# Kernel tuning notes

Hardware: AMD Instinct MI355X
Metric: run time of the kernel (lower is better)

Reference implementation:

```python
import jax, jax.numpy as jnp
import numpy as np

N_NODES = 50000
N_EDGES = 1600000
D_FEAT = 128
ORDER = 2


def setup_inputs() -> dict:
    key = jax.random.key(0)
    k1, k2, k3, k4 = jax.random.split(key, 4)
    x = jax.random.normal(k1, (N_NODES, D_FEAT), dtype=jnp.float32)
    adj_row = jax.random.randint(k2, (N_EDGES,), 0, N_NODES, dtype=jnp.int32)
    adj_col = jax.random.randint(k3, (N_EDGES,), 0, N_NODES, dtype=jnp.int32)
    adj_vals = jax.random.uniform(k4, (N_EDGES,), dtype=jnp.float32)
    return {"x": x, "adj_row": adj_row, "adj_col": adj_col, "adj_vals": adj_vals}


def reference(x, adj_row, adj_col, adj_vals):
    # SGC propagation: x <- A @ x, repeated `order` times.
    # A is sparse COO: A[row, col] = vals; spmm(A, x)[i] = sum_e vals[e]*x[col[e]] into row[e].
    for _ in range(ORDER):
        msgs = adj_vals[:, None] * x[adj_col]          # [E, F] gathered messages
        x = jax.ops.segment_sum(msgs, adj_row, num_segments=N_NODES)  # [N, F]
    return x
```

## Files before the change

### kernel.cpp

```cpp
#include <hip/hip_runtime.h>
#include <hip/hip_fp16.h>

#define N_NODES 50000
#define N_EDGES 1600000
#define D_FEAT  128
#define NB      ((N_NODES + 255) >> 8)

#define P1_WGS   400
#define P1_ROUND 4096
#define P1_CAP   38
#define P2_CAP   14336

__device__ __forceinline__ unsigned short f2bf(float f) {
    union { float f; unsigned u; } v; v.f = f;
    unsigned r = v.u + 0x7fff + ((v.u >> 16) & 1);
    return (unsigned short)(r >> 16);
}
__device__ __forceinline__ float bf_lo(unsigned w) {
    union { unsigned u; float f; } v; v.u = w << 16; return v.f;
}
__device__ __forceinline__ float bf_hi(unsigned w) {
    union { unsigned u; float f; } v; v.u = w & 0xffff0000u; return v.f;
}

__global__ __launch_bounds__(256) void coarse_hist_kernel(
    const int* __restrict__ row, int* __restrict__ gcnt)
{
    __shared__ int s_cnt[NB];
    for (int i = threadIdx.x; i < NB; i += 256) s_cnt[i] = 0;
    __syncthreads();
    int stride = gridDim.x * blockDim.x;
    for (int e = blockIdx.x * blockDim.x + threadIdx.x; e < N_EDGES; e += stride)
        atomicAdd(&s_cnt[row[e] >> 8], 1);
    __syncthreads();
    for (int i = threadIdx.x; i < NB; i += 256)
        if (s_cnt[i]) atomicAdd(&gcnt[i], s_cnt[i]);
}

__global__ __launch_bounds__(256) void bucket_scan_kernel(
    const int* __restrict__ gcnt, int* __restrict__ gbase,
    int* __restrict__ gcur, int* __restrict__ row_ptr)
{
    __shared__ int lds[256];
    int t = threadIdx.x;
    int orig = (t < NB) ? gcnt[t] : 0;
    lds[t] = orig;
    __syncthreads();
    for (int off = 1; off < 256; off <<= 1) {
        int u = (t >= off) ? lds[t - off] : 0;
        __syncthreads();
        lds[t] += u;
        __syncthreads();
    }
    int excl = lds[t] - orig;
    if (t < NB) { gbase[t] = excl; gcur[t] = excl; }
    if (t == 0) row_ptr[N_NODES] = N_EDGES;
}

__global__ __launch_bounds__(256) void p1_bin_kernel(
    const int* __restrict__ row, const int* __restrict__ col,
    const float* __restrict__ val,
    int* __restrict__ gcur, uint2* __restrict__ sedge)
{
    __shared__ uint2    s_buf[NB * P1_CAP];
    __shared__ unsigned s_cnt[NB];
    __shared__ int      s_base[NB];

    int wg = blockIdx.x, t = threadIdx.x;
    int e0 = (int)((long)wg * N_EDGES / P1_WGS);
    int e1 = (int)((long)(wg + 1) * N_EDGES / P1_WGS);

    for (int rbase = e0; rbase < e1; rbase += P1_ROUND) {
        int rend = rbase + P1_ROUND; if (rend > e1) rend = e1;
        for (int i = t; i < NB; i += 256) s_cnt[i] = 0;
        __syncthreads();
        for (int e = rbase + t; e < rend; e += 256) {
            int r = row[e];
            int b = r >> 8;
            uint2 rec;
            rec.x = ((unsigned)r << 16) | (unsigned)col[e];
            rec.y = __float_as_uint(val[e]);
            unsigned pos = atomicAdd(&s_cnt[b], 1u);
            if (pos < P1_CAP) {
                s_buf[b * P1_CAP + pos] = rec;
            } else {
                int gp = atomicAdd(&gcur[b], 1);
                sedge[gp] = rec;
            }
        }
        __syncthreads();
        if (t < NB) {
            int c = (int)s_cnt[t]; if (c > P1_CAP) c = P1_CAP;
            s_base[t] = (c > 0) ? atomicAdd(&gcur[t], c) : 0;
        }
        __syncthreads();
        if (t < NB) {
            int c = (int)s_cnt[t]; if (c > P1_CAP) c = P1_CAP;
            int gb = s_base[t];
            for (int i = 0; i < c; ++i)
                sedge[gb + i] = s_buf[t * P1_CAP + i];
        }
        __syncthreads();
    }
}

__global__ __launch_bounds__(256) void p2_sort_kernel(
    const int* __restrict__ gbase, const int* __restrict__ gcur,
    const uint2* __restrict__ sedge,
    unsigned* __restrict__ spair, int* __restrict__ row_ptr)
{
    __shared__ unsigned s_out[P2_CAP];
    __shared__ int s_cnt[256];
    __shared__ int s_cur[256];

    int b = blockIdx.x, t = threadIdx.x;
    int beg = gbase[b];
    int end = gcur[b];
    int cnt = end - beg;
    int row0 = b << 8;

    s_cnt[t] = 0;
    __syncthreads();
    for (int i = beg + t; i < end; i += 256) {
        int fr = (int)(sedge[i].x >> 16) - row0;
        atomicAdd(&s_cnt[fr], 1);
    }
    __syncthreads();
    int orig = s_cnt[t];
    __syncthreads();
    for (int off = 1; off < 256; off <<= 1) {
        int u = (t >= off) ? s_cnt[t - off] : 0;
        __syncthreads();
        s_cnt[t] += u;
        __syncthreads();
    }
    int excl = s_cnt[t] - orig;
    int r = row0 + t;
    if (r < N_NODES) row_ptr[r] = beg + excl;
    s_cur[t] = excl;
    __syncthreads();

    if (cnt <= P2_CAP) {
        for (int i = beg + t; i < end; i += 256) {
            uint2 rec = sedge[i];
            int fr = (int)(rec.x >> 16) - row0;
            int p = atomicAdd(&s_cur[fr], 1);
            unsigned cv = rec.x & 0xffffu;
            unsigned short hv = __half_as_ushort(__float2half(__uint_as_float(rec.y)));
            s_out[p] = (cv << 16) | (unsigned)hv;
        }
        __syncthreads();
        for (int i = t; i < cnt; i += 256)
            spair[beg + i] = s_out[i];
    } else {
        for (int i = beg + t; i < end; i += 256) {
            uint2 rec = sedge[i];
            int fr = (int)(rec.x >> 16) - row0;
            int p = atomicAdd(&s_cur[fr], 1);
            unsigned cv = rec.x & 0xffffu;
            unsigned short hv = __half_as_ushort(__float2half(__uint_as_float(rec.y)));
            spair[beg + p] = (cv << 16) | (unsigned)hv;
        }
    }
}

__global__ __launch_bounds__(256) void conv_kernel(
    const float2* __restrict__ xin, unsigned* __restrict__ xb)
{
    int t = blockIdx.x * blockDim.x + threadIdx.x;
    if (t < N_NODES * (D_FEAT / 2)) {
        float2 f = xin[t];
        xb[t] = ((unsigned)f2bf(f.y) << 16) | (unsigned)f2bf(f.x);
    }
}

template <bool WRITE_BF16>
__global__ __launch_bounds__(256) void spmm_csr_bf_kernel(
    const int*      __restrict__ row_ptr,
    const unsigned* __restrict__ spair,
    const unsigned* __restrict__ xb,
    unsigned* __restrict__ outb,
    float*    __restrict__ outf)
{
    int group = (blockIdx.x * blockDim.x + threadIdx.x) >> 4;
    int lane  = threadIdx.x & 15;
    if (group >= N_NODES) return;

    int start = row_ptr[group];
    int end   = row_ptr[group + 1];

    float acc[8];
    #pragma unroll
    for (int i = 0; i < 8; ++i) acc[i] = 0.f;

    for (int base = start; base < end; base += 16) {
        int n = end - base; if (n > 16) n = 16;
        int   c = 0;
        float v = 0.f;
        if (lane < n) {
            unsigned rec = spair[base + lane];
            c = (int)(rec >> 16);
            v = __half2float(__ushort_as_half((unsigned short)(rec & 0xffffu)));
        }
        for (int j = 0; j < n; ++j) {
            int   cj = __shfl(c, j, 16);
            float vj = __shfl(v, j, 16);
            uint4 w = *(const uint4*)(xb + (long)cj * (D_FEAT / 2) + lane * 4);
            acc[0] += vj * bf_lo(w.x);
            acc[1] += vj * bf_hi(w.x);
            acc[2] += vj * bf_lo(w.y);
            acc[3] += vj * bf_hi(w.y);
            acc[4] += vj * bf_lo(w.z);
            acc[5] += vj * bf_hi(w.z);
            acc[6] += vj * bf_lo(w.w);
            acc[7] += vj * bf_hi(w.w);
        }
    }

    if (WRITE_BF16) {
        uint4 w;
        w.x = ((unsigned)f2bf(acc[1]) << 16) | (unsigned)f2bf(acc[0]);
        w.y = ((unsigned)f2bf(acc[3]) << 16) | (unsigned)f2bf(acc[2]);
        w.z = ((unsigned)f2bf(acc[5]) << 16) | (unsigned)f2bf(acc[4]);
        w.w = ((unsigned)f2bf(acc[7]) << 16) | (unsigned)f2bf(acc[6]);
        *(uint4*)(outb + (long)group * (D_FEAT / 2) + lane * 4) = w;
    } else {
        float4 a = make_float4(acc[0], acc[1], acc[2], acc[3]);
        float4 b = make_float4(acc[4], acc[5], acc[6], acc[7]);
        float* dst = outf + (long)group * D_FEAT + lane * 8;
        *(float4*)(dst + 0) = a;
        *(float4*)(dst + 4) = b;
    }
}

__global__ __launch_bounds__(256) void spmm_atomic_kernel(
    const int* __restrict__ row, const int* __restrict__ col,
    const float* __restrict__ vals, const float* __restrict__ xin,
    float* __restrict__ xout)
{
    long tid   = (long)blockIdx.x * blockDim.x + threadIdx.x;
    int  edge  = (int)(tid >> 5);
    int  chunk = (int)(tid & 31);
    if (edge >= N_EDGES) return;
    int   r = row[edge];
    int   c = col[edge];
    float v = vals[edge];
    const float4 xv = ((const float4*)(xin + (long)c * D_FEAT))[chunk];
    float* dst = xout + (long)r * D_FEAT + chunk * 4;
    unsafeAtomicAdd(dst + 0, v * xv.x);
    unsafeAtomicAdd(dst + 1, v * xv.y);
    unsafeAtomicAdd(dst + 2, v * xv.z);
    unsafeAtomicAdd(dst + 3, v * xv.w);
}

static inline size_t align_up(size_t x, size_t a) { return (x + a - 1) & ~(a - 1); }

extern "C" void kernel_launch(void* const* d_in, const int* in_sizes, int n_in,
                              void* d_out, int out_size, void* d_ws, size_t ws_size,
                              hipStream_t stream) {
    const float* x        = (const float*)d_in[0];
    const int*   adj_row  = (const int*)d_in[1];
    const int*   adj_col  = (const int*)d_in[2];
    const float* adj_vals = (const float*)d_in[3];
    float*       out      = (float*)d_out;

    const size_t bf_bytes = (size_t)N_NODES * (D_FEAT / 2) * sizeof(unsigned);

    char*     ws      = (char*)d_ws;
    size_t    off     = 0;
    unsigned* xb      = (unsigned*)(ws + off); off = align_up(off + bf_bytes, 512);
    unsigned* tmpb    = (unsigned*)(ws + off); off = align_up(off + bf_bytes, 512);
    uint2*    sedge   = (uint2*)   (ws + off); off = align_up(off + (size_t)N_EDGES * 8, 512);
    unsigned* spair   = (unsigned*)(ws + off); off = align_up(off + (size_t)N_EDGES * 4, 512);
    int*      row_ptr = (int*)     (ws + off); off = align_up(off + (N_NODES + 4) * sizeof(int), 512);
    int*      gcnt    = (int*)     (ws + off); off = align_up(off + NB * sizeof(int), 512);
    int*      gbase   = (int*)     (ws + off); off = align_up(off + NB * sizeof(int), 512);
    int*      gcur    = (int*)     (ws + off); off = align_up(off + NB * sizeof(int), 512);
    const size_t needed = off;

    const int block = 256;

    if (ws_size >= needed) {
        hipMemsetAsync(gcnt, 0, NB * sizeof(int), stream);
        coarse_hist_kernel<<<256, block, 0, stream>>>(adj_row, gcnt);
        bucket_scan_kernel<<<1, block, 0, stream>>>(gcnt, gbase, gcur, row_ptr);
        p1_bin_kernel<<<P1_WGS, block, 0, stream>>>(adj_row, adj_col, adj_vals,
                                                    gcur, sedge);
        p2_sort_kernel<<<NB, block, 0, stream>>>(gbase, gcur, sedge, spair, row_ptr);

        int cgrid = (N_NODES * (D_FEAT / 2) + block - 1) / block;
        conv_kernel<<<cgrid, block, 0, stream>>>((const float2*)x, xb);

        int ngrid = (N_NODES * 16 + block - 1) / block;
        spmm_csr_bf_kernel<true><<<ngrid, block, 0, stream>>>(
            row_ptr, spair, xb, tmpb, (float*)nullptr);
        spmm_csr_bf_kernel<false><<<ngrid, block, 0, stream>>>(
            row_ptr, spair, tmpb, (unsigned*)nullptr, out);
    } else {
        float* tmp = (float*)ws;
        const size_t feat_bytes = (size_t)N_NODES * D_FEAT * sizeof(float);
        hipMemsetAsync(tmp, 0, feat_bytes, stream);
        hipMemsetAsync(out, 0, feat_bytes, stream);
        long total_threads = (long)N_EDGES * 32;
        long grid = (total_threads + block - 1) / block;
        spmm_atomic_kernel<<<dim3((unsigned)grid), dim3(block), 0, stream>>>(
            adj_row, adj_col, adj_vals, x, tmp);
        spmm_atomic_kernel<<<dim3((unsigned)grid), dim3(block), 0, stream>>>(
            adj_row, adj_col, adj_vals, tmp, out);
    }
}
```

Before: 253.2 us.

## Map one wavefront per row in CSR SpMM with 8-way batched gathers

Reworks the CSR SpMM kernel so each row is handled by a full 64-lane wavefront instead of a 16-lane group. Each lane now holds two features and issues a 4-byte load instead of a 16-byte one. The edge loop is unrolled by 8, so several independent gathers are in flight before the accumulation, which is meant to raise memory-level parallelism and hide latency. In exchange it launches four times as many threads, issues narrower loads, and does more shuffles per edge.

New measurement: 239.7 us. -5.3%, faster.

```diff
diff --git a/kernel.cpp b/kernel.cpp
--- a/kernel.cpp
+++ b/kernel.cpp
@@ -182,54 +182,55 @@
     unsigned* __restrict__ outb,
     float*    __restrict__ outf)
 {
-    int group = (blockIdx.x * blockDim.x + threadIdx.x) >> 4;
-    int lane  = threadIdx.x & 15;
-    if (group >= N_NODES) return;
-
-    int start = row_ptr[group];
-    int end   = row_ptr[group + 1];
-
-    float acc[8];
-    #pragma unroll
-    for (int i = 0; i < 8; ++i) acc[i] = 0.f;
-
-    for (int base = start; base < end; base += 16) {
-        int n = end - base; if (n > 16) n = 16;
-        int   c = 0;
-        float v = 0.f;
-        if (lane < n) {
-            unsigned rec = spair[base + lane];
-            c = (int)(rec >> 16);
-            v = __half2float(__ushort_as_half((unsigned short)(rec & 0xffffu)));
-        }
-        for (int j = 0; j < n; ++j) {
-            int   cj = __shfl(c, j, 16);
-            float vj = __shfl(v, j, 16);
-            uint4 w = *(const uint4*)(xb + (long)cj * (D_FEAT / 2) + lane * 4);
-            acc[0] += vj * bf_lo(w.x);
-            acc[1] += vj * bf_hi(w.x);
-            acc[2] += vj * bf_lo(w.y);
-            acc[3] += vj * bf_hi(w.y);
-            acc[4] += vj * bf_lo(w.z);
-            acc[5] += vj * bf_hi(w.z);
-            acc[6] += vj * bf_lo(w.w);
-            acc[7] += vj * bf_hi(w.w);
+    int row  = (blockIdx.x * blockDim.x + threadIdx.x) >> 6;
+    int lane = threadIdx.x & 63;
+    if (row >= N_NODES) return;
+
+    int start = row_ptr[row];
+    int end   = row_ptr[row + 1];
+
+    float acc0 = 0.f, acc1 = 0.f;
+
+    for (int base = start; base < end; base += 64) {
+        int n = end - base; if (n > 64) n = 64;
+        unsigned rec = 0;
+        if (lane < n) rec = spair[base + lane];
+        int   c = (int)(rec >> 16);
+        float v = __half2float(__ushort_as_half((unsigned short)(rec & 0xffffu)));
+
+        int j = 0;
+        for (; j + 8 <= n; j += 8) {
+            int   cc[8];
+            float vv[8];
+            unsigned ww[8];
+            #pragma unroll
+            for (int k = 0; k < 8; ++k) {
+                cc[k] = __shfl(c, j + k, 64);
+                vv[k] = __shfl(v, j + k, 64);
+            }
+            #pragma unroll
+            for (int k = 0; k < 8; ++k)
+                ww[k] = xb[(long)cc[k] * (D_FEAT / 2) + lane];
+            #pragma unroll
+            for (int k = 0; k < 8; ++k) {
+                acc0 += vv[k] * bf_lo(ww[k]);
+                acc1 += vv[k] * bf_hi(ww[k]);
+            }
+        }
+        for (; j < n; ++j) {
+            int   cj = __shfl(c, j, 64);
+            float vj = __shfl(v, j, 64);
+            unsigned w = xb[(long)cj * (D_FEAT / 2) + lane];
+            acc0 += vj * bf_lo(w);
+            acc1 += vj * bf_hi(w);
         }
     }
 
     if (WRITE_BF16) {
-        uint4 w;
-        w.x = ((unsigned)f2bf(acc[1]) << 16) | (unsigned)f2bf(acc[0]);
-        w.y = ((unsigned)f2bf(acc[3]) << 16) | (unsigned)f2bf(acc[2]);
-        w.z = ((unsigned)f2bf(acc[5]) << 16) | (unsigned)f2bf(acc[4]);
-        w.w = ((unsigned)f2bf(acc[7]) << 16) | (unsigned)f2bf(acc[6]);
-        *(uint4*)(outb + (long)group * (D_FEAT / 2) + lane * 4) = w;
+        unsigned w = ((unsigned)f2bf(acc1) << 16) | (unsigned)f2bf(acc0);
+        outb[(long)row * (D_FEAT / 2) + lane] = w;
     } else {
-        float4 a = make_float4(acc[0], acc[1], acc[2], acc[3]);
-        float4 b = make_float4(acc[4], acc[5], acc[6], acc[7]);
-        float* dst = outf + (long)group * D_FEAT + lane * 8;
-        *(float4*)(dst + 0) = a;
-        *(float4*)(dst + 4) = b;
+        *(float2*)(outf + (long)row * D_FEAT + lane * 2) = make_float2(acc0, acc1);
     }
 }
 
@@ -291,7 +292,7 @@
         int cgrid = (N_NODES * (D_FEAT / 2) + block - 1) / block;
         conv_kernel<<<cgrid, block, 0, stream>>>((const float2*)x, xb);
 
-        int ngrid = (N_NODES * 16 + block - 1) / block;
+        int ngrid = (int)(((long)N_NODES * 64 + block - 1) / block);
         spmm_csr_bf_kernel<true><<<ngrid, block, 0, stream>>>(
             row_ptr, spair, xb, tmpb, (float*)nullptr);
         spmm_csr_bf_kernel<false><<<ngrid, block, 0, stream>>>(
```
